# Kernel optimization log

Measured on AMD Instinct MI355X. Metric: run time of the kernel, lower is better.

The kernel has to match this reference:

```python
import jax, jax.numpy as jnp
import numpy as np
from jax import lax

B, T = 8192, 128
HID = 64


def setup_inputs() -> dict:
    key = jax.random.key(0)
    ks = jax.random.split(key, 16)
    actor_ids = jax.random.randint(ks[0], (B, T), 0, 7, dtype=jnp.int32)
    action_ids = jax.random.randint(ks[1], (B, T), 0, 4, dtype=jnp.int32)
    street_ids = jax.random.randint(ks[2], (B, T), 0, 5, dtype=jnp.int32)
    bet_fraction = jax.random.uniform(ks[3], (B, T, 1), dtype=jnp.float32)
    # prefix-valid mask from random lengths (some zero-length rows)
    lengths = jax.random.randint(ks[4], (B,), 0, T + 1)
    valid_mask = jnp.arange(T)[None, :] < lengths[:, None]  # [B,T] bool
    s = 0.1
    params = {
        "E_actor": jax.random.normal(ks[5], (7, 8), jnp.float32) * s,
        "E_action": jax.random.normal(ks[6], (4, 8), jnp.float32) * s,
        "E_street": jax.random.normal(ks[7], (5, 4), jnp.float32) * s,
        "W_proj": jax.random.normal(ks[8], (32, 21), jnp.float32) * s,
        "b_proj": jax.random.normal(ks[9], (32,), jnp.float32) * s,
        "W_ih": jax.random.normal(ks[10], (3 * HID, 32), jnp.float32) * s,
        "W_hh": jax.random.normal(ks[11], (3 * HID, HID), jnp.float32) * s,
        "b_ih": jax.random.normal(ks[12], (3 * HID,), jnp.float32) * s,
        "b_hh": jax.random.normal(ks[13], (3 * HID,), jnp.float32) * s,
    }
    return dict(actor_ids=actor_ids, action_ids=action_ids, street_ids=street_ids,
                bet_fraction=bet_fraction, valid_mask=valid_mask, **params)


def reference(actor_ids, action_ids, street_ids, bet_fraction, valid_mask,
              E_actor, E_action, E_street, W_proj, b_proj,
              W_ih, W_hh, b_ih, b_hh):
    # embed + concat -> [B,T,21]
    feats = jnp.concatenate([E_actor[actor_ids], E_action[action_ids],
                             E_street[street_ids], bet_fraction], axis=-1)
    x = feats @ W_proj.T + b_proj                      # [B,T,32]
    # precompute input-side GRU gates for all timesteps: [B,T,3H]
    xg = x @ W_ih.T + b_ih
    xg_t = jnp.swapaxes(xg, 0, 1)                      # [T,B,3H]
    m_t = jnp.swapaxes(valid_mask, 0, 1)               # [T,B]

    def step(h, inp):
        xg_i, m = inp
        hg = h @ W_hh.T + b_hh                         # [B,3H]
        xr, xz, xn = jnp.split(xg_i, 3, axis=-1)
        hr, hz, hn = jnp.split(hg, 3, axis=-1)
        r = jax.nn.sigmoid(xr + hr)
        z = jax.nn.sigmoid(xz + hz)
        n = jnp.tanh(xn + r * hn)
        h_new = (1.0 - z) * n + z * h
        # only advance hidden state while t < length (prefix-valid mask);
        # final carry equals the GRU hidden at the last valid step, and rows
        # with length 0 stay at the zero init (matches torch masking).
        h = jnp.where(m[:, None], h_new, h)
        return h, None

    h0 = jnp.zeros((x.shape[0], HID), dtype=x.dtype)
    h_final, _ = lax.scan(step, h0, (xg_t, m_t))
    return h_final
```

## Files before the change

### kernel.cpp

```cpp
#include <hip/hip_runtime.h>

#define HID 64
#define TT  128
#define NROWS 8192
#define NGRP (NROWS / 16)

typedef _Float16 half8 __attribute__((ext_vector_type(8)));
typedef float    f32x4 __attribute__((ext_vector_type(4)));

#define WS_WF    0
#define WS_WHH   12288
#define WS_BA    36864
#define WS_BX    37376
#define WS_BH    37632
#define WS_EMB   37888
#define WS_LROW  38176
#define WS_ORDER 70944

__global__ __launch_bounds__(256) void prep(
    const float* __restrict__ E_actor, const float* __restrict__ E_action,
    const float* __restrict__ E_street, const float* __restrict__ W_proj,
    const float* __restrict__ b_proj, const float* __restrict__ W_ih,
    const float* __restrict__ b_ih, const float* __restrict__ W_hh,
    const float* __restrict__ b_hh, const int* __restrict__ mask,
    char* __restrict__ ws)
{
    const int j = threadIdx.x;
    if (blockIdx.x != 0) {
        int* Lrow = (int*)(ws + WS_LROW);
        const int wv = j >> 6, ln = j & 63;
        const int r0 = (blockIdx.x - 1) * 128;
        for (int i = 0; i < 32; i++) {
            const int row = r0 + i * 4 + wv, base = row * TT;
            const int m0 = mask[base + ln], m1 = mask[base + 64 + ln];
            const int L = __popcll(__ballot(m0 != 0)) + __popcll(__ballot(m1 != 0));
            if (ln == 0) Lrow[row] = L;
        }
        return;
    }

    _Float16* WF  = (_Float16*)(ws + WS_WF);
    _Float16* WHH = (_Float16*)(ws + WS_WHH);
    float*    BA  = (float*)(ws + WS_BA);
    float*    BX  = (float*)(ws + WS_BX);
    float*    BH  = (float*)(ws + WS_BH);
    _Float16* EMB = (_Float16*)(ws + WS_EMB);

    __shared__ float wfs[192][32];
    if (j < 192) {
        float wf[21];
        #pragma unroll
        for (int m = 0; m < 21; m++) wf[m] = 0.f;
        float bf = b_ih[j];
        for (int k = 0; k < 32; k++) {
            float w = W_ih[j * 32 + k];
            bf += w * b_proj[k];
            #pragma unroll
            for (int m = 0; m < 21; m++) wf[m] += w * W_proj[k * 21 + m];
        }
        #pragma unroll
        for (int m = 0; m < 21; m++) wfs[j][m] = wf[m];
        #pragma unroll
        for (int m = 21; m < 32; m++) wfs[j][m] = 0.f;
        if (j < 128) BA[j] = bf + b_hh[j];
        else { BX[j - 128] = bf; BH[j - 128] = b_hh[j]; }
    }
    if (j < 17 * 8) {
        int r = j >> 3, m = j & 7;
        float v = 0.f;
        if (r < 7)       v = E_actor[r * 8 + m];
        else if (r < 11) v = E_action[(r - 7) * 8 + m];
        else if (r < 16) v = (m < 4) ? E_street[(r - 11) * 4 + m] : 0.f;
        EMB[j] = (_Float16)v;
    }
    __syncthreads();

    for (int idx = j; idx < 12 * 64; idx += 256) {
        const int T = idx >> 6, lane = idx & 63;
        const int g3 = T >> 2, w = T & 3, m16 = lane & 15, kq = lane >> 4;
        const int jr = g3 * 64 + w * 16 + m16;
        _Float16 v[8];
        #pragma unroll
        for (int m = 0; m < 8; m++) v[m] = (_Float16)wfs[jr][kq * 8 + m];
        *(uint4*)&WF[idx * 8] = *(uint4*)v;
    }
    for (int idx = j; idx < 12 * 2 * 64; idx += 256) {
        const int T = idx >> 7, rem = idx & 127, kt = rem >> 6, lane = rem & 63;
        const int g3 = T >> 2, w = T & 3, m16 = lane & 15, kq = lane >> 4;
        const int jr = g3 * 64 + w * 16 + m16;
        const int kbase = kt * 32 + kq * 8;
        _Float16 v[8];
        #pragma unroll
        for (int m = 0; m < 8; m++) v[m] = (_Float16)W_hh[jr * HID + kbase + m];
        *(uint4*)&WHH[((T * 2 + kt) * 64 + lane) * 8] = *(uint4*)v;
    }
}

__global__ __launch_bounds__(256) void sort_rows(
    const int* __restrict__ Lrow, int* __restrict__ order)
{
    __shared__ int hist[TT + 1];
    __shared__ int pref[TT + 1];
    const int tid = threadIdx.x;
    if (tid <= TT) hist[tid] = 0;
    __syncthreads();
    int rnk[NROWS / 256], Ls[NROWS / 256];
    #pragma unroll 4
    for (int i = 0; i < NROWS / 256; i++) {
        const int r = i * 256 + tid;
        const int L = Lrow[r];
        Ls[i] = L;
        rnk[i] = atomicAdd(&hist[L], 1);
    }
    __syncthreads();
    if (tid == 0) {
        int run = 0;
        for (int i = 0; i <= TT; i++) { pref[i] = run; run += hist[i]; }
    }
    __syncthreads();
    #pragma unroll 4
    for (int i = 0; i < NROWS / 256; i++) {
        const int r = i * 256 + tid;
        order[pref[Ls[i]] + rnk[i]] = r;
    }
}

__global__ __launch_bounds__(256, 2) void gru_mfma(
    const int* __restrict__ actor_ids, const int* __restrict__ action_ids,
    const int* __restrict__ street_ids, const float* __restrict__ bet,
    const char* __restrict__ ws, const int* __restrict__ order,
    const int* __restrict__ Lrow, float* __restrict__ out)
{
    const _Float16* WF  = (const _Float16*)(ws + WS_WF);
    const _Float16* WHH = (const _Float16*)(ws + WS_WHH);
    const float*    BA  = (const float*)(ws + WS_BA);
    const float*    BX  = (const float*)(ws + WS_BX);
    const float*    BH  = (const float*)(ws + WS_BH);
    const _Float16* EMB = (const _Float16*)(ws + WS_EMB);

    __shared__ int2 pb[TT][18];
    __shared__ __align__(16) _Float16 hb[2][16][72];
    __shared__ __align__(16) _Float16 embl[144];

    const int tid = threadIdx.x;
    const int wv  = tid >> 6;
    const int l   = tid & 63;
    const int q   = l >> 4;
    const int n   = l & 15;

    const int b = blockIdx.x;
    const int g = (b & 1) ? (NGRP - 1 - (b >> 1)) : (b >> 1);

    for (int i = tid; i < 136; i += 256) embl[i] = EMB[i];
    for (int i = tid; i < 2 * 16 * 72 / 2; i += 256) ((int*)hb)[i] = 0;
    {
        const int r = tid >> 4, tl = tid & 15;
        const int rowr = order[g * 16 + r];
        const int base = rowr * TT;
        #pragma unroll
        for (int i = 0; i < 8; i++) {
            const int t = tl + 16 * i;
            const int a = actor_ids[base + t], c = action_ids[base + t];
            const int s = street_ids[base + t];
            const float f = bet[base + t];
            pb[t][r] = make_int2(a | (c << 3) | (s << 5), __float_as_int(f));
        }
    }

    half8 Af[3], Ah[3][2];
    #pragma unroll
    for (int g3 = 0; g3 < 3; g3++) {
        const int T = g3 * 4 + wv;
        Af[g3]    = *(const half8*)&WF[(T * 64 + l) * 8];
        Ah[g3][0] = *(const half8*)&WHH[((T * 2 + 0) * 64 + l) * 8];
        Ah[g3][1] = *(const half8*)&WHH[((T * 2 + 1) * 64 + l) * 8];
    }
    f32x4 biasR, biasZ, biasX, biasH;
    #pragma unroll
    for (int e = 0; e < 4; e++) {
        const int idx = 16 * wv + 4 * q + e;
        biasR[e] = BA[idx];
        biasZ[e] = BA[64 + idx];
        biasX[e] = BX[idx];
        biasH[e] = BH[idx];
    }

    const int myrow = order[g * 16 + n];
    const int Ln    = Lrow[myrow];
    const int Lmax  = __shfl(Ln, 15);
    const bool isq2 = (q == 2);

    float h[4] = {0.f, 0.f, 0.f, 0.f};
    const f32x4 zero4 = {0.f, 0.f, 0.f, 0.f};

    __syncthreads();

    f32x4 xR, xZ, xX;
    {
        const int2 p = pb[0][n];
        const int a = p.x & 7, c = (p.x >> 3) & 3, s = (p.x >> 5) & 7;
        const int eidx = (q == 0) ? a : (q == 1) ? (7 + c) : isq2 ? (11 + s) : 16;
        half8 Bf = *(const half8*)&embl[eidx * 8];
        uint4* bu = (uint4*)&Bf;
        _Float16 b2[2] = {(_Float16)__int_as_float(p.y), (_Float16)0.f};
        bu->z = isq2 ? *(unsigned*)b2 : bu->z;
        xR = __builtin_amdgcn_mfma_f32_16x16x32_f16(Af[0], Bf, biasR, 0, 0, 0);
        xZ = __builtin_amdgcn_mfma_f32_16x16x32_f16(Af[1], Bf, biasZ, 0, 0, 0);
        xX = __builtin_amdgcn_mfma_f32_16x16x32_f16(Af[2], Bf, biasX, 0, 0, 0);
    }

    for (int t = 0; t < Lmax; t++) {
        const int buf = t & 1;
        const half8 Bh0 = *(const half8*)&hb[buf][n][q * 8];
        const half8 Bh1 = *(const half8*)&hb[buf][n][32 + q * 8];
        f32x4 aR0 = __builtin_amdgcn_mfma_f32_16x16x32_f16(Ah[0][0], Bh0, xR, 0, 0, 0);
        f32x4 aR1 = __builtin_amdgcn_mfma_f32_16x16x32_f16(Ah[0][1], Bh1, zero4, 0, 0, 0);
        f32x4 aZ0 = __builtin_amdgcn_mfma_f32_16x16x32_f16(Ah[1][0], Bh0, xZ, 0, 0, 0);
        f32x4 aZ1 = __builtin_amdgcn_mfma_f32_16x16x32_f16(Ah[1][1], Bh1, zero4, 0, 0, 0);
        f32x4 aH0 = __builtin_amdgcn_mfma_f32_16x16x32_f16(Ah[2][0], Bh0, biasH, 0, 0, 0);
        f32x4 aH1 = __builtin_amdgcn_mfma_f32_16x16x32_f16(Ah[2][1], Bh1, zero4, 0, 0, 0);
        const f32x4 aXc = xX;

        {
            const int tn = (t + 1 < TT) ? t + 1 : TT - 1;
            const int2 p = pb[tn][n];
            const int a = p.x & 7, c = (p.x >> 3) & 3, s = (p.x >> 5) & 7;
            const int eidx = (q == 0) ? a : (q == 1) ? (7 + c) : isq2 ? (11 + s) : 16;
            half8 Bf = *(const half8*)&embl[eidx * 8];
            uint4* bu = (uint4*)&Bf;
            _Float16 b2[2] = {(_Float16)__int_as_float(p.y), (_Float16)0.f};
            bu->z = isq2 ? *(unsigned*)b2 : bu->z;
            xR = __builtin_amdgcn_mfma_f32_16x16x32_f16(Af[0], Bf, biasR, 0, 0, 0);
            xZ = __builtin_amdgcn_mfma_f32_16x16x32_f16(Af[1], Bf, biasZ, 0, 0, 0);
            xX = __builtin_amdgcn_mfma_f32_16x16x32_f16(Af[2], Bf, biasX, 0, 0, 0);
        }

        const f32x4 aR = aR0 + aR1, aZ = aZ0 + aZ1, aH = aH0 + aH1;
        const bool live = (t < Ln);
        _Float16 hp[4];
        #pragma unroll
        for (int e = 0; e < 4; e++) {
            const float r = __builtin_amdgcn_rcpf(1.f + __expf(-aR[e]));
            const float z = __builtin_amdgcn_rcpf(1.f + __expf(-aZ[e]));
            const float y = aXc[e] + r * aH[e];
            const float nn = 1.f - 2.f * __builtin_amdgcn_rcpf(1.f + __expf(2.f * y));
            const float hv = nn + z * (h[e] - nn);
            h[e] = live ? hv : h[e];
            hp[e] = (_Float16)h[e];
        }
        *(uint2*)&hb[buf ^ 1][n][16 * wv + 4 * q] = *(uint2*)hp;
        __syncthreads();
    }

    float4 o = make_float4(h[0], h[1], h[2], h[3]);
    *(float4*)&out[myrow * HID + 16 * wv + 4 * q] = o;
}

extern "C" void kernel_launch(void* const* d_in, const int* in_sizes, int n_in,
                              void* d_out, int out_size, void* d_ws, size_t ws_size,
                              hipStream_t stream) {
    const int*   actor_ids  = (const int*)d_in[0];
    const int*   action_ids = (const int*)d_in[1];
    const int*   street_ids = (const int*)d_in[2];
    const float* bet        = (const float*)d_in[3];
    const int*   vmask      = (const int*)d_in[4];
    const float* E_actor    = (const float*)d_in[5];
    const float* E_action   = (const float*)d_in[6];
    const float* E_street   = (const float*)d_in[7];
    const float* W_proj     = (const float*)d_in[8];
    const float* b_proj     = (const float*)d_in[9];
    const float* W_ih       = (const float*)d_in[10];
    const float* W_hh       = (const float*)d_in[11];
    const float* b_ih       = (const float*)d_in[12];
    const float* b_hh       = (const float*)d_in[13];
    float*       out        = (float*)d_out;

    char* ws = (char*)d_ws;
    int*  Lrow  = (int*)(ws + WS_LROW);
    int*  order = (int*)(ws + WS_ORDER);

    prep<<<65, 256, 0, stream>>>(E_actor, E_action, E_street, W_proj, b_proj,
                                 W_ih, b_ih, W_hh, b_hh, vmask, ws);
    sort_rows<<<1, 256, 0, stream>>>(Lrow, order);
    gru_mfma<<<NGRP, 256, 0, stream>>>(actor_ids, action_ids, street_ids, bet,
                                       ws, order, Lrow, out);
}
```

Before: 185.1 us.

## Fuse length sort into prep kernel via grid sync; fold log2e into weights

```diff
diff --git a/kernel.cpp b/kernel.cpp
--- a/kernel.cpp
+++ b/kernel.cpp
@@ -4,6 +4,7 @@
 #define TT  128
 #define NROWS 8192
 #define NGRP (NROWS / 16)
+#define LOG2E 1.44269504088896f
 
 typedef _Float16 half8 __attribute__((ext_vector_type(8)));
 typedef float    f32x4 __attribute__((ext_vector_type(4)));
@@ -16,8 +17,12 @@
 #define WS_EMB   37888
 #define WS_LROW  38176
 #define WS_ORDER 70944
-
-__global__ __launch_bounds__(256) void prep(
+#define WS_HIST  103712
+#define WS_PREF  104352
+#define WS_FLAG  104992
+#define WS_DONE  104996
+
+__global__ __launch_bounds__(256) void sortprep(
     const float* __restrict__ E_actor, const float* __restrict__ E_action,
     const float* __restrict__ E_street, const float* __restrict__ W_proj,
     const float* __restrict__ b_proj, const float* __restrict__ W_ih,
@@ -25,104 +30,126 @@
     const float* __restrict__ b_hh, const int* __restrict__ mask,
     char* __restrict__ ws)
 {
-    const int j = threadIdx.x;
-    if (blockIdx.x != 0) {
-        int* Lrow = (int*)(ws + WS_LROW);
-        const int wv = j >> 6, ln = j & 63;
-        const int r0 = (blockIdx.x - 1) * 128;
-        for (int i = 0; i < 32; i++) {
-            const int row = r0 + i * 4 + wv, base = row * TT;
-            const int m0 = mask[base + ln], m1 = mask[base + 64 + ln];
-            const int L = __popcll(__ballot(m0 != 0)) + __popcll(__ballot(m1 != 0));
-            if (ln == 0) Lrow[row] = L;
+    const int tid = threadIdx.x;
+    const int b   = blockIdx.x;
+
+    if (b == 64) {
+        _Float16* WF  = (_Float16*)(ws + WS_WF);
+        _Float16* WHH = (_Float16*)(ws + WS_WHH);
+        float*    BA  = (float*)(ws + WS_BA);
+        float*    BX  = (float*)(ws + WS_BX);
+        float*    BH  = (float*)(ws + WS_BH);
+        _Float16* EMB = (_Float16*)(ws + WS_EMB);
+        __shared__ float wfs[192][32];
+        const int j = tid;
+        if (j < 192) {
+            float wf[21];
+            #pragma unroll
+            for (int m = 0; m < 21; m++) wf[m] = 0.f;
+            float bf = b_ih[j];
+            for (int k = 0; k < 32; k++) {
+                float w = W_ih[j * 32 + k];
+                bf += w * b_proj[k];
+                #pragma unroll
+                for (int m = 0; m < 21; m++) wf[m] += w * W_proj[k * 21 + m];
+            }
+            const float s = (j < 128) ? LOG2E : 2.f * LOG2E;
+            #pragma unroll
+            for (int m = 0; m < 21; m++) wfs[j][m] = wf[m] * s;
+            #pragma unroll
+            for (int m = 21; m < 32; m++) wfs[j][m] = 0.f;
+            if (j < 128) BA[j] = (bf + b_hh[j]) * LOG2E;
+            else { BX[j - 128] = bf * 2.f * LOG2E; BH[j - 128] = b_hh[j] * 2.f * LOG2E; }
+        }
+        if (j < 17 * 8) {
+            int r = j >> 3, m = j & 7;
+            float v = 0.f;
+            if (r < 7)       v = E_actor[r * 8 + m];
+            else if (r < 11) v = E_action[(r - 7) * 8 + m];
+            else if (r < 16) v = (m < 4) ? E_street[(r - 11) * 4 + m] : 0.f;
+            EMB[j] = (_Float16)v;
+        }
+        __syncthreads();
+        for (int idx = j; idx < 12 * 64; idx += 256) {
+            const int T = idx >> 6, lane = idx & 63;
+            const int g3 = T >> 2, w = T & 3, m16 = lane & 15, kq = lane >> 4;
+            const int jr = g3 * 64 + w * 16 + m16;
+            _Float16 v[8];
+            #pragma unroll
+            for (int m = 0; m < 8; m++) v[m] = (_Float16)wfs[jr][kq * 8 + m];
+            *(uint4*)&WF[idx * 8] = *(uint4*)v;
+        }
+        for (int idx = j; idx < 12 * 2 * 64; idx += 256) {
+            const int T = idx >> 7, rem = idx & 127, kt = rem >> 6, lane = rem & 63;
+            const int g3 = T >> 2, w = T & 3, m16 = lane & 15, kq = lane >> 4;
+            const int jr = g3 * 64 + w * 16 + m16;
+            const int kbase = kt * 32 + kq * 8;
+            const float s = (jr < 128) ? LOG2E : 2.f * LOG2E;
+            _Float16 v[8];
+            #pragma unroll
+            for (int m = 0; m < 8; m++) v[m] = (_Float16)(W_hh[jr * HID + kbase + m] * s);
+            *(uint4*)&WHH[((T * 2 + kt) * 64 + lane) * 8] = *(uint4*)v;
         }
         return;
     }
 
-    _Float16* WF  = (_Float16*)(ws + WS_WF);
-    _Float16* WHH = (_Float16*)(ws + WS_WHH);
-    float*    BA  = (float*)(ws + WS_BA);
-    float*    BX  = (float*)(ws + WS_BX);
-    float*    BH  = (float*)(ws + WS_BH);
-    _Float16* EMB = (_Float16*)(ws + WS_EMB);
-
-    __shared__ float wfs[192][32];
-    if (j < 192) {
-        float wf[21];
-        #pragma unroll
-        for (int m = 0; m < 21; m++) wf[m] = 0.f;
-        float bf = b_ih[j];
-        for (int k = 0; k < 32; k++) {
-            float w = W_ih[j * 32 + k];
-            bf += w * b_proj[k];
-            #pragma unroll
-            for (int m = 0; m < 21; m++) wf[m] += w * W_proj[k * 21 + m];
-        }
-        #pragma unroll
-        for (int m = 0; m < 21; m++) wfs[j][m] = wf[m];
-        #pragma unroll
-        for (int m = 21; m < 32; m++) wfs[j][m] = 0.f;
-        if (j < 128) BA[j] = bf + b_hh[j];
-        else { BX[j - 128] = bf; BH[j - 128] = b_hh[j]; }
-    }
-    if (j < 17 * 8) {
-        int r = j >> 3, m = j & 7;
-        float v = 0.f;
-        if (r < 7)       v = E_actor[r * 8 + m];
-        else if (r < 11) v = E_action[(r - 7) * 8 + m];
-        else if (r < 16) v = (m < 4) ? E_street[(r - 11) * 4 + m] : 0.f;
-        EMB[j] = (_Float16)v;
+    int* Lrow  = (int*)(ws + WS_LROW);
+    int* order = (int*)(ws + WS_ORDER);
+    int* hist  = (int*)(ws + WS_HIST);
+    int* pref  = (int*)(ws + WS_PREF);
+    int* flag  = (int*)(ws + WS_FLAG);
+    int* done  = (int*)(ws + WS_DONE);
+
+    __shared__ int sL[128], sR[128];
+    __shared__ int lpref[TT + 1];
+
+    if (b == 0) {
+        for (int i = tid; i <= TT; i += 256) atomicExch(&hist[i], 0);
+        if (tid == 0) atomicExch(done, 0);
+        __syncthreads();
+        if (tid == 0) atomicExch(flag, 1);
+    } else {
+        if (tid == 0) while (atomicAdd(flag, 0) != 1) __builtin_amdgcn_s_sleep(8);
+        __syncthreads();
+    }
+
+    const int wv = tid >> 6, ln = tid & 63;
+    for (int i = 0; i < 32; i++) {
+        const int li  = wv * 32 + i;
+        const int row = b * 128 + li;
+        const int base = row * TT;
+        const int m0 = mask[base + ln], m1 = mask[base + 64 + ln];
+        const int L = __popcll(__ballot(m0 != 0)) + __popcll(__ballot(m1 != 0));
+        if (ln == 0) {
+            Lrow[row] = L;
+            sL[li] = L;
+            sR[li] = atomicAdd(&hist[L], 1);
+        }
     }
     __syncthreads();
-
-    for (int idx = j; idx < 12 * 64; idx += 256) {
-        const int T = idx >> 6, lane = idx & 63;
-        const int g3 = T >> 2, w = T & 3, m16 = lane & 15, kq = lane >> 4;
-        const int jr = g3 * 64 + w * 16 + m16;
-        _Float16 v[8];
-        #pragma unroll
-        for (int m = 0; m < 8; m++) v[m] = (_Float16)wfs[jr][kq * 8 + m];
-        *(uint4*)&WF[idx * 8] = *(uint4*)v;
-    }
-    for (int idx = j; idx < 12 * 2 * 64; idx += 256) {
-        const int T = idx >> 7, rem = idx & 127, kt = rem >> 6, lane = rem & 63;
-        const int g3 = T >> 2, w = T & 3, m16 = lane & 15, kq = lane >> 4;
-        const int jr = g3 * 64 + w * 16 + m16;
-        const int kbase = kt * 32 + kq * 8;
-        _Float16 v[8];
-        #pragma unroll
-        for (int m = 0; m < 8; m++) v[m] = (_Float16)W_hh[jr * HID + kbase + m];
-        *(uint4*)&WHH[((T * 2 + kt) * 64 + lane) * 8] = *(uint4*)v;
-    }
-}
-
-__global__ __launch_bounds__(256) void sort_rows(
-    const int* __restrict__ Lrow, int* __restrict__ order)
-{
-    __shared__ int hist[TT + 1];
-    __shared__ int pref[TT + 1];
-    const int tid = threadIdx.x;
-    if (tid <= TT) hist[tid] = 0;
-    __syncthreads();
-    int rnk[NROWS / 256], Ls[NROWS / 256];
-    #pragma unroll 4
-    for (int i = 0; i < NROWS / 256; i++) {
-        const int r = i * 256 + tid;
-        const int L = Lrow[r];
-        Ls[i] = L;
-        rnk[i] = atomicAdd(&hist[L], 1);
-    }
-    __syncthreads();
-    if (tid == 0) {
-        int run = 0;
-        for (int i = 0; i <= TT; i++) { pref[i] = run; run += hist[i]; }
-    }
-    __syncthreads();
-    #pragma unroll 4
-    for (int i = 0; i < NROWS / 256; i++) {
-        const int r = i * 256 + tid;
-        order[pref[Ls[i]] + rnk[i]] = r;
-    }
+    if (tid == 0) { __threadfence(); atomicAdd(done, 1); }
+
+    if (b == 0) {
+        if (tid == 0) while (atomicAdd(done, 0) != 64) __builtin_amdgcn_s_sleep(8);
+        __syncthreads();
+        if (tid <= TT) lpref[tid] = atomicAdd(&hist[tid], 0);
+        __syncthreads();
+        if (tid == 0) {
+            int run = 0;
+            for (int i = 0; i <= TT; i++) { int t = lpref[i]; lpref[i] = run; run += t; }
+        }
+        __syncthreads();
+        if (tid <= TT) atomicExch(&pref[tid], lpref[tid]);
+        __syncthreads();
+        if (tid == 0) atomicExch(flag, 2);
+    } else {
+        if (tid == 0) while (atomicAdd(flag, 0) != 2) __builtin_amdgcn_s_sleep(8);
+        __syncthreads();
+        if (tid <= TT) lpref[tid] = atomicAdd(&pref[tid], 0);
+        __syncthreads();
+    }
+
+    if (tid < 128) order[lpref[sL[tid]] + sR[tid]] = b * 128 + tid;
 }
 
 __global__ __launch_bounds__(256, 2) void gru_mfma(
@@ -240,10 +267,10 @@
         _Float16 hp[4];
         #pragma unroll
         for (int e = 0; e < 4; e++) {
-            const float r = __builtin_amdgcn_rcpf(1.f + __expf(-aR[e]));
-            const float z = __builtin_amdgcn_rcpf(1.f + __expf(-aZ[e]));
-            const float y = aXc[e] + r * aH[e];
-            const float nn = 1.f - 2.f * __builtin_amdgcn_rcpf(1.f + __expf(2.f * y));
+            const float r = __builtin_amdgcn_rcpf(1.f + __builtin_amdgcn_exp2f(-aR[e]));
+            const float z = __builtin_amdgcn_rcpf(1.f + __builtin_amdgcn_exp2f(-aZ[e]));
+            const float y2 = aXc[e] + r * aH[e];
+            const float nn = 1.f - 2.f * __builtin_amdgcn_rcpf(1.f + __builtin_amdgcn_exp2f(y2));
             const float hv = nn + z * (h[e] - nn);
             h[e] = live ? hv : h[e];
             hp[e] = (_Float16)h[e];
@@ -279,9 +306,8 @@
     int*  Lrow  = (int*)(ws + WS_LROW);
     int*  order = (int*)(ws + WS_ORDER);
 
-    prep<<<65, 256, 0, stream>>>(E_actor, E_action, E_street, W_proj, b_proj,
-                                 W_ih, b_ih, W_hh, b_hh, vmask, ws);
-    sort_rows<<<1, 256, 0, stream>>>(Lrow, order);
+    sortprep<<<65, 256, 0, stream>>>(E_actor, E_action, E_street, W_proj,
+                                     b_proj, W_ih, b_ih, W_hh, b_hh, vmask, ws);
     gru_mfma<<<NGRP, 256, 0, stream>>>(actor_ids, action_ids, street_ids, bet,
                                        ws, order, Lrow, out);
 }
```

Result: no change. 183.7 us (-0.8%).

## Drop length sort, compute row lengths in-kernel, fold log2e into weights

Applied to the files above, without the earlier changes.

```diff
diff --git a/kernel.cpp b/kernel.cpp
--- a/kernel.cpp
+++ b/kernel.cpp
@@ -4,6 +4,7 @@
 #define TT  128
 #define NROWS 8192
 #define NGRP (NROWS / 16)
+#define LOG2E 1.44269504088896f
 
 typedef _Float16 half8 __attribute__((ext_vector_type(8)));
 typedef float    f32x4 __attribute__((ext_vector_type(4)));
@@ -14,31 +15,14 @@
 #define WS_BX    37376
 #define WS_BH    37632
 #define WS_EMB   37888
-#define WS_LROW  38176
-#define WS_ORDER 70944
 
 __global__ __launch_bounds__(256) void prep(
     const float* __restrict__ E_actor, const float* __restrict__ E_action,
     const float* __restrict__ E_street, const float* __restrict__ W_proj,
     const float* __restrict__ b_proj, const float* __restrict__ W_ih,
     const float* __restrict__ b_ih, const float* __restrict__ W_hh,
-    const float* __restrict__ b_hh, const int* __restrict__ mask,
-    char* __restrict__ ws)
+    const float* __restrict__ b_hh, char* __restrict__ ws)
 {
-    const int j = threadIdx.x;
-    if (blockIdx.x != 0) {
-        int* Lrow = (int*)(ws + WS_LROW);
-        const int wv = j >> 6, ln = j & 63;
-        const int r0 = (blockIdx.x - 1) * 128;
-        for (int i = 0; i < 32; i++) {
-            const int row = r0 + i * 4 + wv, base = row * TT;
-            const int m0 = mask[base + ln], m1 = mask[base + 64 + ln];
-            const int L = __popcll(__ballot(m0 != 0)) + __popcll(__ballot(m1 != 0));
-            if (ln == 0) Lrow[row] = L;
-        }
-        return;
-    }
-
     _Float16* WF  = (_Float16*)(ws + WS_WF);
     _Float16* WHH = (_Float16*)(ws + WS_WHH);
     float*    BA  = (float*)(ws + WS_BA);
@@ -47,6 +31,7 @@
     _Float16* EMB = (_Float16*)(ws + WS_EMB);
 
     __shared__ float wfs[192][32];
+    const int j = threadIdx.x;
     if (j < 192) {
         float wf[21];
         #pragma unroll
@@ -58,12 +43,13 @@
             #pragma unroll
             for (int m = 0; m < 21; m++) wf[m] += w * W_proj[k * 21 + m];
         }
-        #pragma unroll
-        for (int m = 0; m < 21; m++) wfs[j][m] = wf[m];
+        const float s = (j < 128) ? LOG2E : 2.f * LOG2E;
+        #pragma unroll
+        for (int m = 0; m < 21; m++) wfs[j][m] = wf[m] * s;
         #pragma unroll
         for (int m = 21; m < 32; m++) wfs[j][m] = 0.f;
-        if (j < 128) BA[j] = bf + b_hh[j];
-        else { BX[j - 128] = bf; BH[j - 128] = b_hh[j]; }
+        if (j < 128) BA[j] = (bf + b_hh[j]) * LOG2E;
+        else { BX[j - 128] = bf * 2.f * LOG2E; BH[j - 128] = b_hh[j] * 2.f * LOG2E; }
     }
     if (j < 17 * 8) {
         int r = j >> 3, m = j & 7;
@@ -89,47 +75,19 @@
         const int g3 = T >> 2, w = T & 3, m16 = lane & 15, kq = lane >> 4;
         const int jr = g3 * 64 + w * 16 + m16;
         const int kbase = kt * 32 + kq * 8;
+        const float s = (jr < 128) ? LOG2E : 2.f * LOG2E;
         _Float16 v[8];
         #pragma unroll
-        for (int m = 0; m < 8; m++) v[m] = (_Float16)W_hh[jr * HID + kbase + m];
+        for (int m = 0; m < 8; m++) v[m] = (_Float16)(W_hh[jr * HID + kbase + m] * s);
         *(uint4*)&WHH[((T * 2 + kt) * 64 + lane) * 8] = *(uint4*)v;
-    }
-}
-
-__global__ __launch_bounds__(256) void sort_rows(
-    const int* __restrict__ Lrow, int* __restrict__ order)
-{
-    __shared__ int hist[TT + 1];
-    __shared__ int pref[TT + 1];
-    const int tid = threadIdx.x;
-    if (tid <= TT) hist[tid] = 0;
-    __syncthreads();
-    int rnk[NROWS / 256], Ls[NROWS / 256];
-    #pragma unroll 4
-    for (int i = 0; i < NROWS / 256; i++) {
-        const int r = i * 256 + tid;
-        const int L = Lrow[r];
-        Ls[i] = L;
-        rnk[i] = atomicAdd(&hist[L], 1);
-    }
-    __syncthreads();
-    if (tid == 0) {
-        int run = 0;
-        for (int i = 0; i <= TT; i++) { pref[i] = run; run += hist[i]; }
-    }
-    __syncthreads();
-    #pragma unroll 4
-    for (int i = 0; i < NROWS / 256; i++) {
-        const int r = i * 256 + tid;
-        order[pref[Ls[i]] + rnk[i]] = r;
     }
 }
 
 __global__ __launch_bounds__(256, 2) void gru_mfma(
     const int* __restrict__ actor_ids, const int* __restrict__ action_ids,
     const int* __restrict__ street_ids, const float* __restrict__ bet,
-    const char* __restrict__ ws, const int* __restrict__ order,
-    const int* __restrict__ Lrow, float* __restrict__ out)
+    const int* __restrict__ mask, const char* __restrict__ ws,
+    float* __restrict__ out)
 {
     const _Float16* WF  = (const _Float16*)(ws + WS_WF);
     const _Float16* WHH = (const _Float16*)(ws + WS_WHH);
@@ -138,9 +96,11 @@
     const float*    BH  = (const float*)(ws + WS_BH);
     const _Float16* EMB = (const _Float16*)(ws + WS_EMB);
 
-    __shared__ int2 pb[TT][18];
+    __shared__ int pb[TT][17];
     __shared__ __align__(16) _Float16 hb[2][16][72];
     __shared__ __align__(16) _Float16 embl[144];
+    __shared__ int part[16][16];
+    __shared__ int Lsh[16];
 
     const int tid = threadIdx.x;
     const int wv  = tid >> 6;
@@ -148,23 +108,25 @@
     const int q   = l >> 4;
     const int n   = l & 15;
 
-    const int b = blockIdx.x;
-    const int g = (b & 1) ? (NGRP - 1 - (b >> 1)) : (b >> 1);
+    const int g = blockIdx.x;
 
     for (int i = tid; i < 136; i += 256) embl[i] = EMB[i];
     for (int i = tid; i < 2 * 16 * 72 / 2; i += 256) ((int*)hb)[i] = 0;
     {
         const int r = tid >> 4, tl = tid & 15;
-        const int rowr = order[g * 16 + r];
-        const int base = rowr * TT;
+        const int base = (g * 16 + r) * TT;
+        int cnt = 0;
         #pragma unroll
         for (int i = 0; i < 8; i++) {
             const int t = tl + 16 * i;
             const int a = actor_ids[base + t], c = action_ids[base + t];
             const int s = street_ids[base + t];
-            const float f = bet[base + t];
-            pb[t][r] = make_int2(a | (c << 3) | (s << 5), __float_as_int(f));
-        }
+            const _Float16 f16 = (_Float16)bet[base + t];
+            const unsigned fb = (unsigned)*(const unsigned short*)&f16;
+            pb[t][r] = (int)(a | (c << 3) | (s << 5) | (fb << 16));
+            cnt += (mask[base + t] != 0);
+        }
+        part[r][tl] = cnt;
     }
 
     half8 Af[3], Ah[3][2];
@@ -185,25 +147,35 @@
         biasH[e] = BH[idx];
     }
 
-    const int myrow = order[g * 16 + n];
-    const int Ln    = Lrow[myrow];
-    const int Lmax  = __shfl(Ln, 15);
+    __syncthreads();
+    if (tid < 16) {
+        int L = 0;
+        #pragma unroll
+        for (int i = 0; i < 16; i++) L += part[tid][i];
+        Lsh[tid] = L;
+    }
+    __syncthreads();
+
+    const int Ln = Lsh[n];
+    int Lmax = Ln;
+    #pragma unroll
+    for (int k = 1; k < 16; k <<= 1) {
+        const int o = __shfl_xor(Lmax, k);
+        Lmax = (o > Lmax) ? o : Lmax;
+    }
+
     const bool isq2 = (q == 2);
-
     float h[4] = {0.f, 0.f, 0.f, 0.f};
     const f32x4 zero4 = {0.f, 0.f, 0.f, 0.f};
 
-    __syncthreads();
-
     f32x4 xR, xZ, xX;
     {
-        const int2 p = pb[0][n];
-        const int a = p.x & 7, c = (p.x >> 3) & 3, s = (p.x >> 5) & 7;
+        const int p = pb[0][n];
+        const int a = p & 7, c = (p >> 3) & 3, s = (p >> 5) & 7;
         const int eidx = (q == 0) ? a : (q == 1) ? (7 + c) : isq2 ? (11 + s) : 16;
         half8 Bf = *(const half8*)&embl[eidx * 8];
         uint4* bu = (uint4*)&Bf;
-        _Float16 b2[2] = {(_Float16)__int_as_float(p.y), (_Float16)0.f};
-        bu->z = isq2 ? *(unsigned*)b2 : bu->z;
+        bu->z = isq2 ? ((unsigned)p >> 16) : bu->z;
         xR = __builtin_amdgcn_mfma_f32_16x16x32_f16(Af[0], Bf, biasR, 0, 0, 0);
         xZ = __builtin_amdgcn_mfma_f32_16x16x32_f16(Af[1], Bf, biasZ, 0, 0, 0);
         xX = __builtin_amdgcn_mfma_f32_16x16x32_f16(Af[2], Bf, biasX, 0, 0, 0);
@@ -223,13 +195,12 @@
 
         {
             const int tn = (t + 1 < TT) ? t + 1 : TT - 1;
-            const int2 p = pb[tn][n];
-            const int a = p.x & 7, c = (p.x >> 3) & 3, s = (p.x >> 5) & 7;
+            const int p = pb[tn][n];
+            const int a = p & 7, c = (p >> 3) & 3, s = (p >> 5) & 7;
             const int eidx = (q == 0) ? a : (q == 1) ? (7 + c) : isq2 ? (11 + s) : 16;
             half8 Bf = *(const half8*)&embl[eidx * 8];
             uint4* bu = (uint4*)&Bf;
-            _Float16 b2[2] = {(_Float16)__int_as_float(p.y), (_Float16)0.f};
-            bu->z = isq2 ? *(unsigned*)b2 : bu->z;
+            bu->z = isq2 ? ((unsigned)p >> 16) : bu->z;
             xR = __builtin_amdgcn_mfma_f32_16x16x32_f16(Af[0], Bf, biasR, 0, 0, 0);
             xZ = __builtin_amdgcn_mfma_f32_16x16x32_f16(Af[1], Bf, biasZ, 0, 0, 0);
             xX = __builtin_amdgcn_mfma_f32_16x16x32_f16(Af[2], Bf, biasX, 0, 0, 0);
@@ -240,10 +211,10 @@
         _Float16 hp[4];
         #pragma unroll
         for (int e = 0; e < 4; e++) {
-            const float r = __builtin_amdgcn_rcpf(1.f + __expf(-aR[e]));
-            const float z = __builtin_amdgcn_rcpf(1.f + __expf(-aZ[e]));
-            const float y = aXc[e] + r * aH[e];
-            const float nn = 1.f - 2.f * __builtin_amdgcn_rcpf(1.f + __expf(2.f * y));
+            const float r = __builtin_amdgcn_rcpf(1.f + __builtin_amdgcn_exp2f(-aR[e]));
+            const float z = __builtin_amdgcn_rcpf(1.f + __builtin_amdgcn_exp2f(-aZ[e]));
+            const float y2 = aXc[e] + r * aH[e];
+            const float nn = 1.f - 2.f * __builtin_amdgcn_rcpf(1.f + __builtin_amdgcn_exp2f(y2));
             const float hv = nn + z * (h[e] - nn);
             h[e] = live ? hv : h[e];
             hp[e] = (_Float16)h[e];
@@ -253,7 +224,7 @@
     }
 
     float4 o = make_float4(h[0], h[1], h[2], h[3]);
-    *(float4*)&out[myrow * HID + 16 * wv + 4 * q] = o;
+    *(float4*)&out[(g * 16 + n) * HID + 16 * wv + 4 * q] = o;
 }
 
 extern "C" void kernel_launch(void* const* d_in, const int* in_sizes, int n_in,
@@ -276,12 +247,8 @@
     float*       out        = (float*)d_out;
 
     char* ws = (char*)d_ws;
-    int*  Lrow  = (int*)(ws + WS_LROW);
-    int*  order = (int*)(ws + WS_ORDER);
-
-    prep<<<65, 256, 0, stream>>>(E_actor, E_action, E_street, W_proj, b_proj,
-                                 W_ih, b_ih, W_hh, b_hh, vmask, ws);
-    sort_rows<<<1, 256, 0, stream>>>(Lrow, order);
+    prep<<<1, 256, 0, stream>>>(E_actor, E_action, E_street, W_proj, b_proj,
+                                W_ih, b_ih, W_hh, b_hh, ws);
     gru_mfma<<<NGRP, 256, 0, stream>>>(actor_ids, action_ids, street_ids, bet,
-                                       ws, order, Lrow, out);
+                                       vmask, ws, out);
 }
```

After: 169.8 us. 1.09x faster.
